# Kernel tuning notes

Hardware: AMD Instinct MI355X
Metric: run time of the kernel (lower is better)

Reference implementation:

```python
import jax, jax.numpy as jnp
import numpy as np

N_NODES = 30000
N_EDGES = 480000
IN_FEATS = 256
H_FEATS = 128
HEADS = 4
OUT_DIM = 128
NEG_SLOPE = 0.2  # PyG GATConv default leaky_relu slope


def gat_conv(x, src, dst, W, att_src, att_dst, bias, concat):
    """PyG-style GATConv (eval mode, self-loops already in src/dst).
    x: [N, Fin]; W: [Fin, H*C]; att_src/att_dst: [H, C]; bias: [H*C] or [C].
    """
    N = x.shape[0]
    H, C = att_src.shape
    h = (x @ W).reshape(N, H, C)                       # [N, H, C]
    a_src = jnp.einsum('nhc,hc->nh', h, att_src)       # [N, H]
    a_dst = jnp.einsum('nhc,hc->nh', h, att_dst)
    e = jax.nn.leaky_relu(a_src[src] + a_dst[dst], NEG_SLOPE)  # [E, H]
    # segment softmax over incoming edges of each dst node
    m = jax.ops.segment_max(e, dst, num_segments=N)    # [N, H]
    m = jnp.where(jnp.isfinite(m), m, 0.0)
    ex = jnp.exp(e - m[dst])
    denom = jax.ops.segment_sum(ex, dst, num_segments=N)
    alpha = ex / denom[dst]                            # [E, H]
    msg = alpha[:, :, None] * h[src]                   # [E, H, C]
    out = jax.ops.segment_sum(msg, dst, num_segments=N)  # [N, H, C]
    if concat:
        out = out.reshape(N, H * C)
    else:
        out = out.mean(axis=1)
    return out + bias


def setup_inputs() -> dict:
    key = jax.random.key(0)
    ks = jax.random.split(key, 12)
    s = 0.05
    x = jax.random.normal(ks[0], (N_NODES, IN_FEATS), dtype=jnp.float32)
    edge_index = jax.random.randint(ks[1], (2, N_EDGES), 0, N_NODES, dtype=jnp.int64)
    W1 = jax.random.normal(ks[2], (IN_FEATS, HEADS * H_FEATS), dtype=jnp.float32) * s
    att_src1 = jax.random.normal(ks[3], (HEADS, H_FEATS), dtype=jnp.float32) * s
    att_dst1 = jax.random.normal(ks[4], (HEADS, H_FEATS), dtype=jnp.float32) * s
    b1 = jnp.zeros((HEADS * H_FEATS,), dtype=jnp.float32)
    W2 = jax.random.normal(ks[5], (HEADS * H_FEATS, HEADS * H_FEATS), dtype=jnp.float32) * s
    att_src2 = jax.random.normal(ks[6], (HEADS, H_FEATS), dtype=jnp.float32) * s
    att_dst2 = jax.random.normal(ks[7], (HEADS, H_FEATS), dtype=jnp.float32) * s
    b2 = jnp.zeros((HEADS * H_FEATS,), dtype=jnp.float32)
    W3 = jax.random.normal(ks[8], (HEADS * H_FEATS, OUT_DIM), dtype=jnp.float32) * s
    att_src3 = jax.random.normal(ks[9], (1, OUT_DIM), dtype=jnp.float32) * s
    att_dst3 = jax.random.normal(ks[10], (1, OUT_DIM), dtype=jnp.float32) * s
    b3 = jnp.zeros((OUT_DIM,), dtype=jnp.float32)
    return {"x": x, "edge_index": edge_index,
            "W1": W1, "att_src1": att_src1, "att_dst1": att_dst1, "b1": b1,
            "W2": W2, "att_src2": att_src2, "att_dst2": att_dst2, "b2": b2,
            "W3": W3, "att_src3": att_src3, "att_dst3": att_dst3, "b3": b3}


def reference(x, edge_index, W1, att_src1, att_dst1, b1,
              W2, att_src2, att_dst2, b2, W3, att_src3, att_dst3, b3):
    # PyG GATConv adds self-loops by default
    loops = jnp.arange(N_NODES, dtype=edge_index.dtype)
    src = jnp.concatenate([edge_index[0], loops])
    dst = jnp.concatenate([edge_index[1], loops])
    h = gat_conv(x, src, dst, W1, att_src1, att_dst1, b1, concat=True)
    h = jax.nn.relu(h)  # dropout inactive in eval mode
    h = gat_conv(h, src, dst, W2, att_src2, att_dst2, b2, concat=True)
    h = jax.nn.relu(h)
    out = gat_conv(h, src, dst, W3, att_src3, att_dst3, b3, concat=False)
    return out
```

## Files before the change

### kernel.cpp

```cpp
#include <hip/hip_runtime.h>


#define NEG_SLOPE 0.2f

typedef __attribute__((ext_vector_type(8))) short short8;
typedef __attribute__((ext_vector_type(4))) float floatx4;

static __device__ __forceinline__ unsigned short f2bf(float f) {
    unsigned u = __float_as_uint(f);
    u = u + 0x7FFFu + ((u >> 16) & 1u);
    return (unsigned short)(u >> 16);
}
static __device__ __forceinline__ float bf2f_lo(unsigned u) {
    return __uint_as_float(u << 16);
}
static __device__ __forceinline__ float bf2f_hi(unsigned u) {
    return __uint_as_float(u & 0xFFFF0000u);
}

static __device__ __forceinline__ void async_copy16(const void* g, void* l) {
    __builtin_amdgcn_global_load_lds(
        (const __attribute__((address_space(1))) unsigned int*)g,
        (__attribute__((address_space(3))) unsigned int*)l, 16, 0, 0);
}


__global__ __launch_bounds__(256)
void cast_bf16_kernel(const float* __restrict__ in, unsigned short* __restrict__ out, int n4) {
    int i = blockIdx.x * 256 + threadIdx.x;
    if (i < n4) {
        float4 v = ((const float4*)in)[i];
        ushort4 o;
        o.x = f2bf(v.x); o.y = f2bf(v.y); o.z = f2bf(v.z); o.w = f2bf(v.w);
        ((ushort4*)out)[i] = o;
    }
}

__global__ __launch_bounds__(256)
void wt_kernel(const float* __restrict__ W, unsigned short* __restrict__ WT, int K, int N) {
    int idx = blockIdx.x * 256 + threadIdx.x;
    if (idx < K * N) {
        int k = idx / N, n = idx - k * N;
        WT[(size_t)n * K + k] = f2bf(W[idx]);
    }
}


__global__ __launch_bounds__(256)
void init_counts_kernel(int* cursor, int N) {
    int i = blockIdx.x * 256 + threadIdx.x;
    if (i < N) cursor[i] = 1;
}

__global__ __launch_bounds__(256)
void hist_kernel(const int* __restrict__ ei, int* cursor, int E) {
    int e = blockIdx.x * 256 + threadIdx.x;
    if (e < E) atomicAdd(&cursor[ei[E + e]], 1);
}

__global__ __launch_bounds__(1024)
void scan_bsum_kernel(const int* __restrict__ cursor, int* __restrict__ bsum, int N) {
    __shared__ int wsum[16];
    int tid = threadIdx.x, lane = tid & 63, w = tid >> 6;
    int i = blockIdx.x * 1024 + tid;
    int v = (i < N) ? cursor[i] : 0;
    #pragma unroll
    for (int off = 32; off; off >>= 1) v += __shfl_xor(v, off, 64);
    if (lane == 0) wsum[w] = v;
    __syncthreads();
    if (tid == 0) {
        int t = 0;
        #pragma unroll
        for (int k = 0; k < 16; ++k) t += wsum[k];
        bsum[blockIdx.x] = t;
    }
}

__global__ __launch_bounds__(64)
void scan_boffs_kernel(const int* __restrict__ bsum, int* __restrict__ boffs,
                       int NB, int* __restrict__ row_ptr, int N) {
    int lane = threadIdx.x;
    int v = (lane < NB) ? bsum[lane] : 0;
    int x = v;
    #pragma unroll
    for (int off = 1; off < 64; off <<= 1) {
        int t = __shfl_up(x, off, 64);
        if (lane >= off) x += t;
    }
    if (lane < NB) boffs[lane] = x - v;
    if (lane == 63) row_ptr[N] = x;
}

__global__ __launch_bounds__(1024)
void scan_final_kernel(int* __restrict__ cursor, const int* __restrict__ boffs,
                       int* __restrict__ row_ptr, int N) {
    __shared__ int wsum[16];
    int tid = threadIdx.x, lane = tid & 63, w = tid >> 6;
    int i = blockIdx.x * 1024 + tid;
    int v = (i < N) ? cursor[i] : 0;
    int x = v;
    #pragma unroll
    for (int off = 1; off < 64; off <<= 1) {
        int t = __shfl_up(x, off, 64);
        if (lane >= off) x += t;
    }
    if (lane == 63) wsum[w] = x;
    __syncthreads();
    if (w == 0 && lane < 16) {
        int y = wsum[lane];
        #pragma unroll
        for (int off = 1; off < 16; off <<= 1) {
            int t = __shfl_up(y, off, 64);
            if (lane >= off) y += t;
        }
        wsum[lane] = y;
    }
    __syncthreads();
    int woff = (w == 0) ? 0 : wsum[w - 1];
    int ex = boffs[blockIdx.x] + woff + x - v;
    if (i < N) { row_ptr[i] = ex; cursor[i] = ex; }
}

__global__ __launch_bounds__(256)
void scatter_kernel(const int* __restrict__ ei, int* cursor,
                    int* __restrict__ csr_src, int E, int N) {
    int i = blockIdx.x * 256 + threadIdx.x;
    if (i < E) {
        int s = ei[i], d = ei[E + i];
        int pos = atomicAdd(&cursor[d], 1);
        csr_src[pos] = s;
    } else if (i < E + N) {
        int n = i - E;
        int pos = atomicAdd(&cursor[n], 1);
        csr_src[pos] = n;
    }
}


__global__ __launch_bounds__(256)
void mfma_gemm_kernel(const unsigned short* __restrict__ A,
                      const unsigned short* __restrict__ BT,
                      unsigned short* __restrict__ C,
                      const float* __restrict__ att_src,
                      const float* __restrict__ att_dst,
                      float* __restrict__ a_srcO, float* __restrict__ a_dstO,
                      int H, int M, int Nn, int K) {
    __shared__ unsigned short As[128 * 32];
    __shared__ unsigned short Bs[128 * 32];
    __shared__ float psum[2][128];
    __shared__ float pdsum[2][128];
    const int tid = threadIdx.x;
    const int m0 = blockIdx.y * 128;
    const int n0 = blockIdx.x * 128;
    const int head = blockIdx.x;
    const int lane = tid & 63, wave = tid >> 6;
    const int wm = (wave & 1) * 64, wn = (wave >> 1) * 64;
    const int quad = lane >> 4, rr = lane & 15;

    const int r16 = lane >> 2;
    const int phys = lane & 3;
    const int rowL0 = wave * 32 + r16;
    const int rowL1 = wave * 32 + 16 + r16;
    const int seg0 = phys ^ ((rowL0 >> 1) & 3);
    const int seg1 = phys ^ ((rowL1 >> 1) & 3);
    const int gmA0 = min(m0 + rowL0, M - 1);
    const int gmA1 = min(m0 + rowL1, M - 1);
    const int gnB0 = n0 + rowL0;
    const int gnB1 = n0 + rowL1;
    unsigned short* ldsA0 = As + (wave * 32) * 32;
    unsigned short* ldsA1 = As + (wave * 32 + 16) * 32;
    unsigned short* ldsB0 = Bs + (wave * 32) * 32;
    unsigned short* ldsB1 = Bs + (wave * 32 + 16) * 32;

    const int swz = quad ^ ((rr >> 1) & 3);

    floatx4 acc[4][4] = {};

    for (int k0 = 0; k0 < K; k0 += 32) {
        async_copy16(A  + (size_t)gmA0 * K + k0 + seg0 * 8, ldsA0);
        async_copy16(A  + (size_t)gmA1 * K + k0 + seg1 * 8, ldsA1);
        async_copy16(BT + (size_t)gnB0 * K + k0 + seg0 * 8, ldsB0);
        async_copy16(BT + (size_t)gnB1 * K + k0 + seg1 * 8, ldsB1);
        __syncthreads();

        short8 af[4], bf[4];
        #pragma unroll
        for (int mi = 0; mi < 4; ++mi)
            af[mi] = *(const short8*)(As + (wm + mi * 16 + rr) * 32 + swz * 8);
        #pragma unroll
        for (int ni = 0; ni < 4; ++ni)
            bf[ni] = *(const short8*)(Bs + (wn + ni * 16 + rr) * 32 + swz * 8);
        #pragma unroll
        for (int mi = 0; mi < 4; ++mi)
            #pragma unroll
            for (int ni = 0; ni < 4; ++ni)
                acc[mi][ni] = __builtin_amdgcn_mfma_f32_16x16x32_bf16(
                    af[mi], bf[ni], acc[mi][ni], 0, 0, 0);
        __syncthreads();
    }

    #pragma unroll
    for (int mi = 0; mi < 4; ++mi) {
        #pragma unroll
        for (int ni = 0; ni < 4; ++ni) {
            int col = n0 + wn + ni * 16 + rr;
            #pragma unroll
            for (int r = 0; r < 4; ++r) {
                int row = m0 + wm + mi * 16 + quad * 4 + r;
                if (row < M) C[(size_t)row * Nn + col] = f2bf(acc[mi][ni][r]);
            }
        }
    }

    float ats[4], atd[4];
    #pragma unroll
    for (int ni = 0; ni < 4; ++ni) {
        int c = wn + ni * 16 + rr;
        ats[ni] = att_src[head * 128 + c];
        atd[ni] = att_dst[head * 128 + c];
    }
    const int wnh = wn >> 6;
    #pragma unroll
    for (int mi = 0; mi < 4; ++mi) {
        #pragma unroll
        for (int r = 0; r < 4; ++r) {
            float ps = 0.f, pd = 0.f;
            #pragma unroll
            for (int ni = 0; ni < 4; ++ni) {
                ps += ats[ni] * acc[mi][ni][r];
                pd += atd[ni] * acc[mi][ni][r];
            }
            #pragma unroll
            for (int off = 1; off < 16; off <<= 1) {
                ps += __shfl_xor(ps, off, 64);
                pd += __shfl_xor(pd, off, 64);
            }
            if (rr == 0) {
                int row = wm + mi * 16 + quad * 4 + r;
                psum[wnh][row] = ps;
                pdsum[wnh][row] = pd;
            }
        }
    }
    __syncthreads();
    if (tid < 128) {
        int gr = m0 + tid;
        if (gr < M) {
            a_srcO[(size_t)gr * H + head] = psum[0][tid] + psum[1][tid];
            a_dstO[(size_t)gr * H + head] = pdsum[0][tid] + pdsum[1][tid];
        }
    }
}


template<int F, int H, bool RELU, bool BF16OUT>
__global__ __launch_bounds__(256)
void agg_kernel(const unsigned* __restrict__ hfeat, const float* __restrict__ a_src,
                const float* __restrict__ a_dst, const int* __restrict__ row_ptr,
                const int* __restrict__ csr_src, const float* __restrict__ bias,
                void* __restrict__ out_v, int N) {
    constexpr int C = 128;
    constexpr int UPL = F / 128;
    constexpr int RU = F / 2;
    const int wave = threadIdx.x >> 6, lane = threadIdx.x & 63;
    const int n = blockIdx.x * 4 + wave;
    if (n >= N) return;
    const int begin = __builtin_amdgcn_readfirstlane(row_ptr[n]);
    const int deg = __builtin_amdgcn_readfirstlane(row_ptr[n + 1]) - begin;
    const int myh = (2 * UPL * lane) / C;
    const float adst = a_dst[n * H + myh];

    float acc[2 * UPL];
    #pragma unroll
    for (int j = 0; j < 2 * UPL; ++j) acc[j] = 0.f;
    float dacc = 0.f;

    unsigned u0[UPL], u1[UPL], u2[UPL], u3[UPL];
    float av0 = 0.f, av1 = 0.f, av2 = 0.f, av3 = 0.f;

#define LOADSLOT(idx, U, AV)                                              \
    {                                                                     \
        int s_ = __builtin_amdgcn_readfirstlane(csr_src[begin + (idx)]);  \
        if (UPL == 4) {                                                   \
            uint4 t_ = ((const uint4*)(hfeat + (size_t)s_ * RU))[lane];   \
            U[0] = t_.x; U[1] = t_.y; U[2] = t_.z; U[3] = t_.w;           \
        } else {                                                          \
            U[0] = hfeat[(size_t)s_ * RU + lane];                         \
        }                                                                 \
        AV = a_src[s_ * H + myh];                                         \
    }

#define CONSUME(U, AV)                                                    \
    {                                                                     \
        float e_ = AV + adst;                                             \
        e_ = e_ > 0.f ? e_ : NEG_SLOPE * e_;                              \
        float ex_ = __expf(e_);                                           \
        dacc += ex_;                                                      \
        _Pragma("unroll")                                                 \
        for (int q_ = 0; q_ < UPL; ++q_) {                                \
            acc[2 * q_]     += ex_ * bf2f_lo(U[q_]);                      \
            acc[2 * q_ + 1] += ex_ * bf2f_hi(U[q_]);                      \
        }                                                                 \
    }

    LOADSLOT(0, u0, av0);
    if (deg > 1) LOADSLOT(1, u1, av1);
    if (deg > 2) LOADSLOT(2, u2, av2);
    if (deg > 3) LOADSLOT(3, u3, av3);
    int i = 0;
    for (; i + 8 <= deg; i += 4) {
        CONSUME(u0, av0); LOADSLOT(i + 4, u0, av0);
        CONSUME(u1, av1); LOADSLOT(i + 5, u1, av1);
        CONSUME(u2, av2); LOADSLOT(i + 6, u2, av2);
        CONSUME(u3, av3); LOADSLOT(i + 7, u3, av3);
    }
    int rem = deg - i;
    CONSUME(u0, av0); if (rem > 4) LOADSLOT(i + 4, u0, av0);
    if (rem > 1) { CONSUME(u1, av1); if (rem > 5) LOADSLOT(i + 5, u1, av1); }
    if (rem > 2) { CONSUME(u2, av2); if (rem > 6) LOADSLOT(i + 6, u2, av2); }
    if (rem > 3) CONSUME(u3, av3);
    if (rem > 4) CONSUME(u0, av0);
    if (rem > 5) CONSUME(u1, av1);
    if (rem > 6) CONSUME(u2, av2);
#undef LOADSLOT
#undef CONSUME

    float inv = 1.f / dacc;
    const int cb = 2 * UPL * lane;
    if (BF16OUT) {
        unsigned pk[UPL];
        #pragma unroll
        for (int q = 0; q < UPL; ++q) {
            float v0 = acc[2 * q] * inv + bias[cb + 2 * q];
            float v1 = acc[2 * q + 1] * inv + bias[cb + 2 * q + 1];
            if (RELU) { v0 = fmaxf(v0, 0.f); v1 = fmaxf(v1, 0.f); }
            pk[q] = (unsigned)f2bf(v0) | ((unsigned)f2bf(v1) << 16);
        }
        if (UPL == 4) {
            uint4 t; t.x = pk[0]; t.y = pk[1]; t.z = pk[2]; t.w = pk[3];
            ((uint4*)((unsigned*)out_v + (size_t)n * RU))[lane] = t;
        } else {
            ((unsigned*)out_v)[(size_t)n * RU + lane] = pk[0];
        }
    } else {
        #pragma unroll
        for (int q = 0; q < UPL; ++q) {
            float v0 = acc[2 * q] * inv + bias[cb + 2 * q];
            float v1 = acc[2 * q + 1] * inv + bias[cb + 2 * q + 1];
            if (RELU) { v0 = fmaxf(v0, 0.f); v1 = fmaxf(v1, 0.f); }
            float2 o; o.x = v0; o.y = v1;
            ((float2*)((float*)out_v + (size_t)n * F))[UPL * lane + q] = o;
        }
    }
}


extern "C" void kernel_launch(void* const* d_in, const int* in_sizes, int n_in,
                              void* d_out, int out_size, void* d_ws, size_t ws_size,
                              hipStream_t stream) {
    const float* x        = (const float*)d_in[0];
    const int*   ei       = (const int*)  d_in[1];
    const float* W1       = (const float*)d_in[2];
    const float* att_src1 = (const float*)d_in[3];
    const float* att_dst1 = (const float*)d_in[4];
    const float* b1       = (const float*)d_in[5];
    const float* W2       = (const float*)d_in[6];
    const float* att_src2 = (const float*)d_in[7];
    const float* att_dst2 = (const float*)d_in[8];
    const float* b2       = (const float*)d_in[9];
    const float* W3       = (const float*)d_in[10];
    const float* att_src3 = (const float*)d_in[11];
    const float* att_dst3 = (const float*)d_in[12];
    const float* b3       = (const float*)d_in[13];

    const int IN_FEATS = 256;
    const int N = in_sizes[0] / IN_FEATS;
    const int E = in_sizes[1] / 2;
    const int ET = E + N;
    const int NB = (N + 1023) / 1024;

    char* p = (char*)d_ws;
    unsigned short* h_bf    = (unsigned short*)p; p += (size_t)N * 512 * sizeof(unsigned short);
    unsigned short* act_bf  = (unsigned short*)p; p += (size_t)N * 512 * sizeof(unsigned short);
    unsigned short* x_bf    = (unsigned short*)p; p += (size_t)N * 256 * sizeof(unsigned short);
    float*          a_src   = (float*)p;          p += (size_t)N * 4 * sizeof(float);
    float*          a_dst   = (float*)p;          p += (size_t)N * 4 * sizeof(float);
    unsigned short* W_T     = (unsigned short*)p; p += (size_t)512 * 512 * sizeof(unsigned short);
    int*            row_ptr = (int*)p;            p += ((size_t)N + 16) * sizeof(int);
    int*            cursor  = (int*)p;            p += ((size_t)N + 16) * sizeof(int);
    int*            bsum    = (int*)p;            p += 64 * sizeof(int);
    int*            boffs   = (int*)p;            p += 64 * sizeof(int);
    int*            csr_src = (int*)p;            p += (size_t)ET * sizeof(int);

    init_counts_kernel<<<(N + 255) / 256, 256, 0, stream>>>(cursor, N);
    hist_kernel<<<(E + 255) / 256, 256, 0, stream>>>(ei, cursor, E);
    scan_bsum_kernel<<<NB, 1024, 0, stream>>>(cursor, bsum, N);
    scan_boffs_kernel<<<1, 64, 0, stream>>>(bsum, boffs, NB, row_ptr, N);
    scan_final_kernel<<<NB, 1024, 0, stream>>>(cursor, boffs, row_ptr, N);
    scatter_kernel<<<(E + N + 255) / 256, 256, 0, stream>>>(ei, cursor, csr_src, E, N);

    {
        int n4 = N * 256 / 4;
        cast_bf16_kernel<<<(n4 + 255) / 256, 256, 0, stream>>>(x, x_bf, n4);
    }

    const int MB = (N + 127) / 128;
    const int NB4 = (N + 3) / 4;

    wt_kernel<<<(256 * 512 + 255) / 256, 256, 0, stream>>>(W1, W_T, 256, 512);
    mfma_gemm_kernel<<<dim3(4, MB), 256, 0, stream>>>(x_bf, W_T, h_bf, att_src1, att_dst1, a_src, a_dst, 4, N, 512, 256);
    agg_kernel<512, 4, true, true><<<NB4, 256, 0, stream>>>((const unsigned*)h_bf, a_src, a_dst, row_ptr, csr_src, b1, act_bf, N);

    wt_kernel<<<(512 * 512 + 255) / 256, 256, 0, stream>>>(W2, W_T, 512, 512);
    mfma_gemm_kernel<<<dim3(4, MB), 256, 0, stream>>>(act_bf, W_T, h_bf, att_src2, att_dst2, a_src, a_dst, 4, N, 512, 512);
    agg_kernel<512, 4, true, true><<<NB4, 256, 0, stream>>>((const unsigned*)h_bf, a_src, a_dst, row_ptr, csr_src, b2, act_bf, N);

    wt_kernel<<<(512 * 128 + 255) / 256, 256, 0, stream>>>(W3, W_T, 512, 128);
    mfma_gemm_kernel<<<dim3(1, MB), 256, 0, stream>>>(act_bf, W_T, h_bf, att_src3, att_dst3, a_src, a_dst, 1, N, 128, 512);
    agg_kernel<128, 1, false, false><<<NB4, 256, 0, stream>>>((const unsigned*)h_bf, a_src, a_dst, row_ptr, csr_src, b3, d_out, N);
}
```

Before: 422.5 us.

## Load GEMM fragments directly from global into registers with double buffering

The MFMA GEMM no longer stages A and B tiles through LDS with async copies and two barriers per k-step. Each lane now loads its bf16 fragments straight from global memory into registers, using two register sets so the next k-slice loads while the current MFMAs run. This is meant to remove barrier and LDS round-trip overhead. In exchange, waves that share rows rely on L1/L2 for reuse instead of LDS. The loop also assumes an even number of 32-wide k-steps; otherwise the final pass consumes stale fragments.

Measured after the change: 465.7 us. 10.2% more time.

```diff
diff --git a/kernel.cpp b/kernel.cpp
--- a/kernel.cpp
+++ b/kernel.cpp
@@ -16,12 +16,6 @@
 }
 static __device__ __forceinline__ float bf2f_hi(unsigned u) {
     return __uint_as_float(u & 0xFFFF0000u);
-}
-
-static __device__ __forceinline__ void async_copy16(const void* g, void* l) {
-    __builtin_amdgcn_global_load_lds(
-        (const __attribute__((address_space(1))) unsigned int*)g,
-        (__attribute__((address_space(3))) unsigned int*)l, 16, 0, 0);
 }
 
 
@@ -145,8 +139,6 @@
                       const float* __restrict__ att_dst,
                       float* __restrict__ a_srcO, float* __restrict__ a_dstO,
                       int H, int M, int Nn, int K) {
-    __shared__ unsigned short As[128 * 32];
-    __shared__ unsigned short Bs[128 * 32];
     __shared__ float psum[2][128];
     __shared__ float pdsum[2][128];
     const int tid = threadIdx.x;
@@ -157,47 +149,44 @@
     const int wm = (wave & 1) * 64, wn = (wave >> 1) * 64;
     const int quad = lane >> 4, rr = lane & 15;
 
-    const int r16 = lane >> 2;
-    const int phys = lane & 3;
-    const int rowL0 = wave * 32 + r16;
-    const int rowL1 = wave * 32 + 16 + r16;
-    const int seg0 = phys ^ ((rowL0 >> 1) & 3);
-    const int seg1 = phys ^ ((rowL1 >> 1) & 3);
-    const int gmA0 = min(m0 + rowL0, M - 1);
-    const int gmA1 = min(m0 + rowL1, M - 1);
-    const int gnB0 = n0 + rowL0;
-    const int gnB1 = n0 + rowL1;
-    unsigned short* ldsA0 = As + (wave * 32) * 32;
-    unsigned short* ldsA1 = As + (wave * 32 + 16) * 32;
-    unsigned short* ldsB0 = Bs + (wave * 32) * 32;
-    unsigned short* ldsB1 = Bs + (wave * 32 + 16) * 32;
-
-    const int swz = quad ^ ((rr >> 1) & 3);
+    const unsigned short* Ap[4];
+    const unsigned short* Bp[4];
+    #pragma unroll
+    for (int mi = 0; mi < 4; ++mi)
+        Ap[mi] = A + (size_t)min(m0 + wm + mi * 16 + rr, M - 1) * K + quad * 8;
+    #pragma unroll
+    for (int ni = 0; ni < 4; ++ni)
+        Bp[ni] = BT + (size_t)(n0 + wn + ni * 16 + rr) * K + quad * 8;
 
     floatx4 acc[4][4] = {};
-
-    for (int k0 = 0; k0 < K; k0 += 32) {
-        async_copy16(A  + (size_t)gmA0 * K + k0 + seg0 * 8, ldsA0);
-        async_copy16(A  + (size_t)gmA1 * K + k0 + seg1 * 8, ldsA1);
-        async_copy16(BT + (size_t)gnB0 * K + k0 + seg0 * 8, ldsB0);
-        async_copy16(BT + (size_t)gnB1 * K + k0 + seg1 * 8, ldsB1);
-        __syncthreads();
-
-        short8 af[4], bf[4];
-        #pragma unroll
-        for (int mi = 0; mi < 4; ++mi)
-            af[mi] = *(const short8*)(As + (wm + mi * 16 + rr) * 32 + swz * 8);
-        #pragma unroll
-        for (int ni = 0; ni < 4; ++ni)
-            bf[ni] = *(const short8*)(Bs + (wn + ni * 16 + rr) * 32 + swz * 8);
-        #pragma unroll
-        for (int mi = 0; mi < 4; ++mi)
-            #pragma unroll
-            for (int ni = 0; ni < 4; ++ni)
-                acc[mi][ni] = __builtin_amdgcn_mfma_f32_16x16x32_bf16(
-                    af[mi], bf[ni], acc[mi][ni], 0, 0, 0);
-        __syncthreads();
-    }
+    short8 a0[4], b0[4], a1[4], b1[4];
+
+#define LOADF(AF, BF, k0)                                                     \
+    { _Pragma("unroll")                                                       \
+      for (int q = 0; q < 4; ++q) AF[q] = *(const short8*)(Ap[q] + (k0));     \
+      _Pragma("unroll")                                                       \
+      for (int q = 0; q < 4; ++q) BF[q] = *(const short8*)(Bp[q] + (k0)); }
+
+#define MFMAS(AF, BF)                                                         \
+    { _Pragma("unroll")                                                       \
+      for (int mi = 0; mi < 4; ++mi)                                          \
+          _Pragma("unroll")                                                   \
+          for (int ni = 0; ni < 4; ++ni)                                      \
+              acc[mi][ni] = __builtin_amdgcn_mfma_f32_16x16x32_bf16(          \
+                  AF[mi], BF[ni], acc[mi][ni], 0, 0, 0); }
+
+    LOADF(a0, b0, 0);
+    const int nk = K >> 5;
+    int k = 0;
+    for (int c = 0; c < nk; c += 2) {
+        if (c + 1 < nk) LOADF(a1, b1, k + 32);
+        MFMAS(a0, b0);
+        if (c + 2 < nk) LOADF(a0, b0, k + 64);
+        MFMAS(a1, b1);
+        k += 64;
+    }
+#undef LOADF
+#undef MFMAS
 
     #pragma unroll
     for (int mi = 0; mi < 4; ++mi) {
```

## Split 512-wide aggregation across heads with one wave per node-head slice

Applied to the files above, without the earlier changes.

Replaces the per-node aggregation for the two 4-head layers with a kernel where each wave handles one head (64 lanes × 2 bf16) of one node, so a node's four heads run in separate waves and blocks. Each lane loads a single dword per edge instead of a uint4, and the block index maps slot bits to head and node. The aim is more parallelism and latency hiding in the gather-bound phase, at the cost of four times as many index and a_src reads per edge and narrower memory transactions.

Result: slower. 454.0 us (+7.4%).

```diff
diff --git a/kernel.cpp b/kernel.cpp
--- a/kernel.cpp
+++ b/kernel.cpp
@@ -253,13 +253,82 @@
 }
 
 
+template<bool RELU>
+__global__ __launch_bounds__(256)
+void agg_slice_kernel(const unsigned* __restrict__ hfeat, const float* __restrict__ a_src,
+                      const float* __restrict__ a_dst, const int* __restrict__ row_ptr,
+                      const int* __restrict__ csr_src, const float* __restrict__ bias,
+                      unsigned* __restrict__ out, int N) {
+    constexpr int RU = 256;
+    const int wave = threadIdx.x >> 6, lane = threadIdx.x & 63;
+    const int slot = blockIdx.x & 7;
+    const int head = slot & 3;
+    const int n = (blockIdx.x >> 3) * 8 + wave * 2 + (slot >> 2);
+    if (n >= N) return;
+    const int begin = __builtin_amdgcn_readfirstlane(row_ptr[n]);
+    const int deg = __builtin_amdgcn_readfirstlane(row_ptr[n + 1]) - begin;
+    const float adst = a_dst[n * 4 + head];
+    const unsigned* hsl = hfeat + head * 64 + lane;
+
+    float acc0 = 0.f, acc1 = 0.f, dacc = 0.f;
+    unsigned u0 = 0, u1 = 0, u2 = 0, u3 = 0;
+    float av0 = 0.f, av1 = 0.f, av2 = 0.f, av3 = 0.f;
+
+#define LOADSLOT(idx, U, AV)                                              \
+    {                                                                     \
+        int s_ = __builtin_amdgcn_readfirstlane(csr_src[begin + (idx)]);  \
+        U = hsl[(size_t)s_ * RU];                                         \
+        AV = a_src[s_ * 4 + head];                                        \
+    }
+
+#define CONSUME(U, AV)                                                    \
+    {                                                                     \
+        float e_ = AV + adst;                                             \
+        e_ = e_ > 0.f ? e_ : NEG_SLOPE * e_;                              \
+        float ex_ = __expf(e_);                                           \
+        dacc += ex_;                                                      \
+        acc0 += ex_ * bf2f_lo(U);                                         \
+        acc1 += ex_ * bf2f_hi(U);                                         \
+    }
+
+    LOADSLOT(0, u0, av0);
+    if (deg > 1) LOADSLOT(1, u1, av1);
+    if (deg > 2) LOADSLOT(2, u2, av2);
+    if (deg > 3) LOADSLOT(3, u3, av3);
+    int i = 0;
+    for (; i + 8 <= deg; i += 4) {
+        CONSUME(u0, av0); LOADSLOT(i + 4, u0, av0);
+        CONSUME(u1, av1); LOADSLOT(i + 5, u1, av1);
+        CONSUME(u2, av2); LOADSLOT(i + 6, u2, av2);
+        CONSUME(u3, av3); LOADSLOT(i + 7, u3, av3);
+    }
+    int rem = deg - i;
+    CONSUME(u0, av0); if (rem > 4) LOADSLOT(i + 4, u0, av0);
+    if (rem > 1) { CONSUME(u1, av1); if (rem > 5) LOADSLOT(i + 5, u1, av1); }
+    if (rem > 2) { CONSUME(u2, av2); if (rem > 6) LOADSLOT(i + 6, u2, av2); }
+    if (rem > 3) CONSUME(u3, av3);
+    if (rem > 4) CONSUME(u0, av0);
+    if (rem > 5) CONSUME(u1, av1);
+    if (rem > 6) CONSUME(u2, av2);
+#undef LOADSLOT
+#undef CONSUME
+
+    float inv = 1.f / dacc;
+    int c = head * 128 + 2 * lane;
+    float v0 = acc0 * inv + bias[c];
+    float v1 = acc1 * inv + bias[c + 1];
+    if (RELU) { v0 = fmaxf(v0, 0.f); v1 = fmaxf(v1, 0.f); }
+    out[(size_t)n * RU + head * 64 + lane] =
+        (unsigned)f2bf(v0) | ((unsigned)f2bf(v1) << 16);
+}
+
+
 template<int F, int H, bool RELU, bool BF16OUT>
 __global__ __launch_bounds__(256)
 void agg_kernel(const unsigned* __restrict__ hfeat, const float* __restrict__ a_src,
                 const float* __restrict__ a_dst, const int* __restrict__ row_ptr,
                 const int* __restrict__ csr_src, const float* __restrict__ bias,
                 void* __restrict__ out_v, int N) {
-    constexpr int C = 128;
     constexpr int UPL = F / 128;
     constexpr int RU = F / 2;
     const int wave = threadIdx.x >> 6, lane = threadIdx.x & 63;
@@ -267,7 +336,7 @@
     if (n >= N) return;
     const int begin = __builtin_amdgcn_readfirstlane(row_ptr[n]);
     const int deg = __builtin_amdgcn_readfirstlane(row_ptr[n + 1]) - begin;
-    const int myh = (2 * UPL * lane) / C;
+    const int myh = (2 * UPL * lane) / 128;
     const float adst = a_dst[n * H + myh];
 
     float acc[2 * UPL];
@@ -406,14 +475,15 @@
 
     const int MB = (N + 127) / 128;
     const int NB4 = (N + 3) / 4;
+    const int NSL = ((N + 7) / 8) * 8;
 
     wt_kernel<<<(256 * 512 + 255) / 256, 256, 0, stream>>>(W1, W_T, 256, 512);
     mfma_gemm_kernel<<<dim3(4, MB), 256, 0, stream>>>(x_bf, W_T, h_bf, att_src1, att_dst1, a_src, a_dst, 4, N, 512, 256);
-    agg_kernel<512, 4, true, true><<<NB4, 256, 0, stream>>>((const unsigned*)h_bf, a_src, a_dst, row_ptr, csr_src, b1, act_bf, N);
+    agg_slice_kernel<true><<<NSL, 256, 0, stream>>>((const unsigned*)h_bf, a_src, a_dst, row_ptr, csr_src, b1, (unsigned*)act_bf, N);
 
     wt_kernel<<<(512 * 512 + 255) / 256, 256, 0, stream>>>(W2, W_T, 512, 512);
     mfma_gemm_kernel<<<dim3(4, MB), 256, 0, stream>>>(act_bf, W_T, h_bf, att_src2, att_dst2, a_src, a_dst, 4, N, 512, 512);
-    agg_kernel<512, 4, true, true><<<NB4, 256, 0, stream>>>((const unsigned*)h_bf, a_src, a_dst, row_ptr, csr_src, b2, act_bf, N);
+    agg_slice_kernel<true><<<NSL, 256, 0, stream>>>((const unsigned*)h_bf, a_src, a_dst, row_ptr, csr_src, b2, (unsigned*)act_bf, N);
 
     wt_kernel<<<(512 * 128 + 255) / 256, 256, 0, stream>>>(W3, W_T, 512, 128);
     mfma_gemm_kernel<<<dim3(1, MB), 256, 0, stream>>>(act_bf, W_T, h_bf, att_src3, att_dst3, a_src, a_dst, 1, N, 128, 512);
```
